# Optimization experiments

Measured on AMD Instinct MI355X. Metric: run time of the kernel, lower is better.

Reference implementation:

```python
import jax, jax.numpy as jnp
import numpy as np

# Deformable DETR encoder layer constants (match init_kwargs / input_specs)
SPATIAL_SHAPES = [(100, 152), (50, 76), (25, 38), (13, 19)]  # (H, W) per level
D_MODEL, D_FFN = 256, 1024
N_LEVELS, N_HEADS, N_POINTS = 4, 8, 4
HEAD_DIM = D_MODEL // N_HEADS
LEN_IN = sum(h * w for h, w in SPATIAL_SHAPES)  # 20197
BATCH = 2


def layer_norm(x, g, b, eps=1e-5):
    m = x.mean(-1, keepdims=True)
    v = ((x - m) ** 2).mean(-1, keepdims=True)
    return (x - m) * jax.lax.rsqrt(v + eps) * g + b


def sample_level(value_l, loc, H, W):
    # value_l: [B, nH, H*W, d]; loc: [B, nH, N, 2] normalized to [0,1]
    # Bilinear sampling, align_corners=False, zero padding (torch grid_sample semantics)
    x = loc[..., 0] * W - 0.5
    y = loc[..., 1] * H - 0.5
    x0, y0 = jnp.floor(x), jnp.floor(y)
    out = jnp.zeros(loc.shape[:-1] + (value_l.shape[-1],), value_l.dtype)
    for dx, dy in ((0, 0), (1, 0), (0, 1), (1, 1)):
        xi, yi = x0 + dx, y0 + dy
        w = (1.0 - jnp.abs(x - xi)) * (1.0 - jnp.abs(y - yi))
        valid = (xi >= 0) & (xi < W) & (yi >= 0) & (yi < H)
        idx = (jnp.clip(yi, 0, H - 1) * W + jnp.clip(xi, 0, W - 1)).astype(jnp.int32)
        v = jnp.take_along_axis(value_l, idx[..., None], axis=2)  # [B,nH,N,d]
        out = out + v * (w * valid.astype(value_l.dtype))[..., None]
    return out


def ms_deform_attn(query, src, ref, W_off, b_off, W_attn, b_attn, W_val, b_val, W_out, b_out):
    B, Lq, C = query.shape
    # value projection -> [B, nH, Len_in, head_dim]
    value = (src @ W_val + b_val).reshape(B, LEN_IN, N_HEADS, HEAD_DIM).transpose(0, 2, 1, 3)
    off = (query @ W_off + b_off).reshape(B, Lq, N_HEADS, N_LEVELS, N_POINTS, 2)
    attn = (query @ W_attn + b_attn).reshape(B, Lq, N_HEADS, N_LEVELS * N_POINTS)
    attn = jax.nn.softmax(attn, -1).reshape(B, Lq, N_HEADS, N_LEVELS, N_POINTS)
    # offset normalizer is (W, H) per level
    normalizer = jnp.array([[w, h] for h, w in SPATIAL_SHAPES], dtype=query.dtype)
    loc = ref[:, :, None, :, None, :] + off / normalizer[None, None, None, :, None, :]  # [B,Lq,nH,nL,nP,2]
    out = jnp.zeros((B, N_HEADS, Lq, HEAD_DIM), query.dtype)
    start = 0
    for l, (H, W) in enumerate(SPATIAL_SHAPES):
        v_l = value[:, :, start:start + H * W]
        start += H * W
        loc_l = loc[:, :, :, l].transpose(0, 2, 1, 3, 4).reshape(B, N_HEADS, Lq * N_POINTS, 2)
        s = sample_level(v_l, loc_l, H, W).reshape(B, N_HEADS, Lq, N_POINTS, HEAD_DIM)
        a = attn[:, :, :, l].transpose(0, 2, 1, 3)  # [B,nH,Lq,nP]
        out = out + (s * a[..., None]).sum(3)
    out = out.transpose(0, 2, 1, 3).reshape(B, Lq, C)
    return out @ W_out + b_out


def setup_inputs() -> dict:
    key = jax.random.key(0)
    ks = jax.random.split(key, 20)
    s = 0.02
    spatial_shapes = jnp.array(SPATIAL_SHAPES, dtype=jnp.int64)
    lsi = np.cumsum([0] + [h * w for h, w in SPATIAL_SHAPES[:-1]])
    return {
        'src': jax.random.normal(ks[0], (BATCH, LEN_IN, D_MODEL), jnp.float32),
        'pos': jax.random.normal(ks[1], (BATCH, LEN_IN, D_MODEL), jnp.float32),
        'reference_points': jax.random.uniform(ks[2], (BATCH, LEN_IN, N_LEVELS, 2), jnp.float32),
        'spatial_shapes': spatial_shapes,
        'level_start_index': jnp.array(lsi, dtype=jnp.int64),
        'W_off': jax.random.normal(ks[3], (D_MODEL, N_HEADS * N_LEVELS * N_POINTS * 2), jnp.float32) * s,
        'b_off': jax.random.normal(ks[4], (N_HEADS * N_LEVELS * N_POINTS * 2,), jnp.float32) * s,
        'W_attn': jax.random.normal(ks[5], (D_MODEL, N_HEADS * N_LEVELS * N_POINTS), jnp.float32) * s,
        'b_attn': jnp.zeros((N_HEADS * N_LEVELS * N_POINTS,), jnp.float32),
        'W_val': jax.random.normal(ks[6], (D_MODEL, D_MODEL), jnp.float32) * s,
        'b_val': jnp.zeros((D_MODEL,), jnp.float32),
        'W_out': jax.random.normal(ks[7], (D_MODEL, D_MODEL), jnp.float32) * s,
        'b_out': jnp.zeros((D_MODEL,), jnp.float32),
        'W1': jax.random.normal(ks[8], (D_MODEL, D_FFN), jnp.float32) * s,
        'b1': jnp.zeros((D_FFN,), jnp.float32),
        'W2': jax.random.normal(ks[9], (D_FFN, D_MODEL), jnp.float32) * s,
        'b2': jnp.zeros((D_MODEL,), jnp.float32),
        'g1': jnp.ones((D_MODEL,), jnp.float32),
        'be1': jnp.zeros((D_MODEL,), jnp.float32),
        'g2': jnp.ones((D_MODEL,), jnp.float32),
        'be2': jnp.zeros((D_MODEL,), jnp.float32),
    }


def reference(src, pos, reference_points, spatial_shapes, level_start_index,
              W_off, b_off, W_attn, b_attn, W_val, b_val, W_out, b_out,
              W1, b1, W2, b2, g1, be1, g2, be2):
    # eval mode: all dropouts are identity; ReLUDropout -> relu
    query = src + pos
    src2 = ms_deform_attn(query, src, reference_points,
                          W_off, b_off, W_attn, b_attn, W_val, b_val, W_out, b_out)
    x = layer_norm(src + src2, g1, be1)
    ffn = jax.nn.relu(x @ W1 + b1) @ W2 + b2
    return layer_norm(x + ffn, g2, be2)
```

## Files before the change

kernel.cpp:

```cpp
#include <hip/hip_runtime.h>
#include <math.h>

#define LEN_IN_C 20197
#define BATCH_C 2
#define BL_C (BATCH_C * LEN_IN_C)

typedef short  bf16x8 __attribute__((ext_vector_type(8)));
typedef float  f32x4  __attribute__((ext_vector_type(4)));

__device__ __forceinline__ ushort f2bf(float f) {
    unsigned u = __float_as_uint(f);
    return (ushort)((u + 0x7fffu + ((u >> 16) & 1u)) >> 16);
}
__device__ __forceinline__ float bf2f(ushort u) {
    return __uint_as_float((uint)u << 16);
}
__device__ __forceinline__ uint pkbf(float a, float b) {
    uint r;
    asm("v_cvt_pk_bf16_f32 %0, %1, %2" : "=v"(r) : "v"(a), "v"(b));
    return r;
}
__device__ __forceinline__ void dot2bf(float& a, uint v, uint w) {
    asm("v_dot2_f32_bf16 %0, %1, %2, %0" : "+v"(a) : "v"(v), "v"(w));
}
__device__ __forceinline__ void gload16(const void* g, void* l) {
    __builtin_amdgcn_global_load_lds(
        (const __attribute__((address_space(1))) unsigned char*)g,
        (__attribute__((address_space(3))) unsigned char*)l, 16, 0, 0);
}
__device__ __forceinline__ int xcd_swz(int lid, int nwg) {
    const int q = nwg >> 3, r = nwg & 7;
    const int xcd = lid & 7, p = lid >> 3;
    return (xcd < r ? xcd * (q + 1) : r * (q + 1) + (xcd - r) * q) + p;
}

__device__ __forceinline__ void tcast32(
    const float* W, ushort* WT, int K, int N, int n0, int k0, float* tile )
{
    const int ty = threadIdx.x >> 3, tx = threadIdx.x & 7;
    float4 v = *(const float4*)(W + (size_t)(k0 + ty) * N + n0 + tx * 4);
    tile[ty * 33 + tx * 4 + 0] = v.x; tile[ty * 33 + tx * 4 + 1] = v.y;
    tile[ty * 33 + tx * 4 + 2] = v.z; tile[ty * 33 + tx * 4 + 3] = v.w;
    __syncthreads();
    ushort4 o;
    o.x = f2bf(tile[(tx * 4 + 0) * 33 + ty]);
    o.y = f2bf(tile[(tx * 4 + 1) * 33 + ty]);
    o.z = f2bf(tile[(tx * 4 + 2) * 33 + ty]);
    o.w = f2bf(tile[(tx * 4 + 3) * 33 + ty]);
    *(ushort4*)(WT + (size_t)(n0 + ty) * K + k0 + tx * 4) = o;
}

__global__ __launch_bounds__(256) void prep_all(
    const float* __restrict__ src, const float* __restrict__ pos,
    const float* __restrict__ Wv, const float* __restrict__ Wo,
    const float* __restrict__ Wa, const float* __restrict__ Wout,
    const float* __restrict__ W1, const float* __restrict__ W2,
    const float* __restrict__ bo, const float* __restrict__ ba,
    ushort* __restrict__ Tval, ushort* __restrict__ Toa,
    ushort* __restrict__ Tout, ushort* __restrict__ TW1,
    ushort* __restrict__ TW2, float* __restrict__ boa,
    ushort* __restrict__ qout, ushort* __restrict__ srcb)
{
    __shared__ float tile[32 * 33];
    const int bx = blockIdx.x;
    const int tid = threadIdx.x;
    if (bx < 64) {
        tcast32(Wv, Tval, 256, 256, (bx & 7) * 32, (bx >> 3) * 32, tile);
    } else if (bx < 128) {
        const int s = bx - 64;
        tcast32(Wout, Tout, 256, 256, (s & 7) * 32, (s >> 3) * 32, tile);
    } else if (bx < 384) {
        const int s = bx - 128;
        tcast32(W1, TW1, 256, 1024, (s & 31) * 32, (s >> 5) * 32, tile);
    } else if (bx < 640) {
        const int s = bx - 384;
        tcast32(W2, TW2, 1024, 256, (s & 7) * 32, (s >> 3) * 32, tile);
    } else if (bx < 736) {
        const int idx = (bx - 640) * 256 + tid;
        const int n = idx >> 6, k4 = (idx & 63) * 4;
        ushort4 o; ushort* po = (ushort*)&o;
        #pragma unroll
        for (int j = 0; j < 4; ++j) {
            const int k = k4 + j;
            const float v = (n < 256) ? Wo[(size_t)k * 256 + n]
                                      : Wa[(size_t)k * 128 + (n - 256)];
            po[j] = f2bf(v);
        }
        *(ushort4*)(Toa + (size_t)n * 256 + k4) = o;
    } else if (bx < 738) {
        const int n = (bx - 736) * 256 + tid;
        if (n < 384) boa[n] = (n < 256) ? bo[n] : ba[n - 256];
    } else {
        const int n8 = BL_C * 32;
        for (int i = (bx - 738) * 256 + tid; i < n8; i += 1024 * 256) {
            const size_t base = (size_t)i * 8;
            float4 a0 = *(const float4*)(src + base);
            float4 a1 = *(const float4*)(src + base + 4);
            float4 b0 = *(const float4*)(pos + base);
            float4 b1 = *(const float4*)(pos + base + 4);
            uint4 o;
            o.x = pkbf(a0.x + b0.x, a0.y + b0.y);
            o.y = pkbf(a0.z + b0.z, a0.w + b0.w);
            o.z = pkbf(a1.x + b1.x, a1.y + b1.y);
            o.w = pkbf(a1.z + b1.z, a1.w + b1.w);
            *(uint4*)(qout + base) = o;
            uint4 s4;
            s4.x = pkbf(a0.x, a0.y); s4.y = pkbf(a0.z, a0.w);
            s4.z = pkbf(a1.x, a1.y); s4.w = pkbf(a1.z, a1.w);
            *(uint4*)(srcb + base) = s4;
        }
    }
}

template <bool RELU>
__device__ __forceinline__ void gemm_core(
    ushort* lsB, const int lid,
    const ushort* __restrict__ A, const ushort* __restrict__ BT,
    const float* __restrict__ bias, ushort* __restrict__ C,
    const int M, const int N, const int K, const int NT, const int nwg)
{
    const int nid = xcd_swz(lid, nwg);
    const int nt = nid % NT, mt = nid / NT;
    const int row0 = mt * 128, col0 = nt * 64;

    const int tid = threadIdx.x;
    const int ln = tid & 63, wv = tid >> 6;
    const int l16 = ln & 15, lk = ln >> 4;

    uint abase[2];
    #pragma unroll
    for (int m = 0; m < 2; ++m) {
        int rr = row0 + wv * 32 + m * 16 + l16;
        if (rr > M - 1) rr = M - 1;
        abase[m] = (uint)rr * K + lk * 8;
    }
    uint bbase[4], bxor[4];
    #pragma unroll
    for (int n = 0; n < 4; ++n) {
        const int brow = n * 16 + l16;
        bbase[n] = (uint)(brow * 256 + lk * 16);
        bxor[n]  = (uint)((brow & 7) << 4);
    }

    f32x4 acc[2][4] = {};
    const int nch = K >> 7;

    for (int ch = 0; ch < nch; ++ch) {
        const int kc0 = ch << 7;

        bf16x8 ar[4][2];
        #pragma unroll
        for (int s = 0; s < 4; ++s)
            #pragma unroll
            for (int m = 0; m < 2; ++m)
                ar[s][m] = *(const bf16x8*)(A + abase[m] + kc0 + s * 32);

        if (ch) __syncthreads();
        #pragma unroll
        for (int j = 0; j < 4; ++j) {
            const int d = j * 256 + tid;
            const int brow = d >> 4;
            const int c = (d & 15) ^ (brow & 7);
            gload16(BT + (size_t)(col0 + brow) * K + kc0 + c * 8,
                    (char*)lsB + j * 4096 + wv * 1024);
        }
        __syncthreads();

        #pragma unroll
        for (int gs = 0; gs < 4; ++gs) {
            bf16x8 bv[4];
            #pragma unroll
            for (int n = 0; n < 4; ++n)
                bv[n] = *(const bf16x8*)((const char*)lsB +
                        ((bbase[n] + gs * 64) ^ bxor[n]));
            #pragma unroll
            for (int m = 0; m < 2; ++m)
                #pragma unroll
                for (int n = 0; n < 4; ++n)
                    acc[m][n] = __builtin_amdgcn_mfma_f32_16x16x32_bf16(
                        bv[n], ar[gs][m], acc[m][n], 0, 0, 0);
        }
    }

    #pragma unroll
    for (int m = 0; m < 2; ++m) {
        const int grow = row0 + wv * 32 + m * 16 + l16;
        if (grow >= M) continue;
        ushort* crow = C + (size_t)grow * N;
        #pragma unroll
        for (int n = 0; n < 4; ++n) {
            const int col4 = col0 + n * 16 + lk * 4;
            float4 bs = *(const float4*)(bias + col4);
            f32x4 v = acc[m][n];
            float o0 = v[0] + bs.x, o1 = v[1] + bs.y, o2 = v[2] + bs.z, o3 = v[3] + bs.w;
            if (RELU) {
                o0 = fmaxf(o0, 0.f); o1 = fmaxf(o1, 0.f);
                o2 = fmaxf(o2, 0.f); o3 = fmaxf(o3, 0.f);
            }
            *(uint2*)(crow + col4) = make_uint2(pkbf(o0, o1), pkbf(o2, o3));
        }
    }
}

template <bool RELU>
__global__ __launch_bounds__(256) void gemm_bs(
    const ushort* __restrict__ A, const ushort* __restrict__ BT,
    const float* __restrict__ bias, ushort* __restrict__ C,
    const int M, const int N, const int K, const int NT, const int nwg)
{
    __shared__ ushort lsB[64 * 128];
    gemm_core<RELU>(lsB, blockIdx.x, A, BT, bias, C, M, N, K, NT, nwg);
}

__global__ __launch_bounds__(256) void gemm_dual(
    const ushort* __restrict__ A1, const ushort* __restrict__ BT1,
    const float* __restrict__ b1, ushort* __restrict__ C1,
    const int N1, const int NT1, const int nwg1,
    const ushort* __restrict__ A2, const ushort* __restrict__ BT2,
    const float* __restrict__ b2, ushort* __restrict__ C2,
    const int N2, const int NT2, const int nwg2)
{
    __shared__ ushort lsB[64 * 128];
    if ((int)blockIdx.x < nwg1)
        gemm_core<false>(lsB, blockIdx.x, A1, BT1, b1, C1, BL_C, N1, 256, NT1, nwg1);
    else
        gemm_core<false>(lsB, blockIdx.x - nwg1, A2, BT2, b2, C2, BL_C, N2, 256, NT2, nwg2);
}

__global__ __launch_bounds__(256) void sample_kernel(
    const ushort* __restrict__ value,
    const ushort* __restrict__ oa,
    const float* __restrict__ ref,
    ushort* __restrict__ outbf)
{
    constexpr int Hs[4] = {100, 50, 25, 13};
    constexpr int Ws[4] = {152, 76, 38, 19};
    constexpr int St[4] = {0, 15200, 19000, 19950};
    constexpr int NWG = (BL_C + 7) / 8;

    const int bq0 = xcd_swz(blockIdx.x, NWG) * 8;
    const int t = threadIdx.x;

    __shared__ uint2 s_pw[8][8][33];

    #pragma unroll
    for (int rnd = 0; rnd < 4; ++rnd) {
        const int qi2 = t >> 7, r2 = t & 127;
        const int qloc = rnd * 2 + qi2;
        int bq = bq0 + qloc; if (bq > BL_C - 1) bq = BL_C - 1;
        const int b = (bq >= LEN_IN_C) ? 1 : 0;
        const int h = r2 >> 4, i = r2 & 15, l = i >> 2, p = i & 3;
        const ushort* crow = oa + (size_t)bq * 384;

        float lg = bf2f(crow[256 + h * 16 + i]);
        float mx = lg;
        #pragma unroll
        for (int o = 1; o < 16; o <<= 1) mx = fmaxf(mx, __shfl_xor(mx, o, 16));
        float e = __expf(lg - mx), sm = e;
        #pragma unroll
        for (int o = 1; o < 16; o <<= 1) sm += __shfl_xor(sm, o, 16);
        const float aw = e / sm;

        const uint ov = *(const uint*)(crow + h * 32 + l * 8 + p * 2);
        const float ox = __uint_as_float(ov << 16);
        const float oy = __uint_as_float(ov & 0xffff0000u);
        const float2 rxy = *(const float2*)(ref + (size_t)bq * 8 + l * 2);
        const int H = Hs[l], W = Ws[l];
        const float x = rxy.x * (float)W + ox - 0.5f;
        const float y = rxy.y * (float)H + oy - 0.5f;
        const float x0f = floorf(x), y0f = floorf(y);
        const float fx = x - x0f, fy = y - y0f;
        const int x0 = (int)x0f, y0 = (int)y0f;

        const float wx0 = (x0 >= 0 && x0 < W) ? (1.f - fx) : 0.f;
        const float wx1 = (x0 + 1 >= 0 && x0 + 1 < W) ? fx : 0.f;
        int xb = x0 < 0 ? 0 : (x0 > W - 2 ? W - 2 : x0);
        float wLx = (xb == x0) ? wx0 : ((xb == x0 + 1) ? wx1 : 0.f);
        float wRx = (xb + 1 == x0 + 1) ? wx1 : ((xb + 1 == x0) ? wx0 : 0.f);
        wLx *= aw; wRx *= aw;

        const uint rowb = (uint)(b * LEN_IN_C + St[l] + xb);
        #pragma unroll
        for (int dy = 0; dy < 2; ++dy) {
            const int yy = y0 + dy;
            const bool vy = (yy >= 0) & (yy < H);
            const float wy = vy ? (dy ? fy : 1.f - fy) : 0.f;
            const int yc = yy < 0 ? 0 : (yy > H - 1 ? H - 1 : yy);
            const uint off = (rowb + (uint)(yc * W)) * 512u;
            s_pw[qloc][h][i * 2 + dy] = make_uint2(off, pkbf(wRx * wy, wLx * wy));
        }
    }
    __syncthreads();

    const int q = t >> 5, h2 = (t >> 2) & 7, d4 = t & 3;
    int bq = bq0 + q; if (bq > BL_C - 1) bq = BL_C - 1;
    const char* vb = (const char*)value;
    const uint toff = (uint)(h2 * 64 + d4 * 16);

    float a0 = 0.f, a1 = 0.f, a2 = 0.f, a3 = 0.f;
    float a4 = 0.f, a5 = 0.f, a6 = 0.f, a7 = 0.f;
    #pragma unroll 4
    for (int j = 0; j < 32; ++j) {
        const uint2 pw = s_pw[q][h2][j];
        const char* p = vb + (size_t)(pw.x + toff);
        const uint4 v0 = *(const uint4*)p;
        const uint4 v1 = *(const uint4*)(p + 512);
        const uint w = pw.y;
        dot2bf(a0, __builtin_amdgcn_perm(v0.x, v1.x, 0x05040100u), w);
        dot2bf(a1, __builtin_amdgcn_perm(v0.x, v1.x, 0x07060302u), w);
        dot2bf(a2, __builtin_amdgcn_perm(v0.y, v1.y, 0x05040100u), w);
        dot2bf(a3, __builtin_amdgcn_perm(v0.y, v1.y, 0x07060302u), w);
        dot2bf(a4, __builtin_amdgcn_perm(v0.z, v1.z, 0x05040100u), w);
        dot2bf(a5, __builtin_amdgcn_perm(v0.z, v1.z, 0x07060302u), w);
        dot2bf(a6, __builtin_amdgcn_perm(v0.w, v1.w, 0x05040100u), w);
        dot2bf(a7, __builtin_amdgcn_perm(v0.w, v1.w, 0x07060302u), w);
    }
    uint4 o;
    o.x = pkbf(a0, a1); o.y = pkbf(a2, a3);
    o.z = pkbf(a4, a5); o.w = pkbf(a6, a7);
    *(uint4*)(outbf + (size_t)bq * 256 + h2 * 32 + d4 * 8) = o;
}

template <bool ABF, bool OF32>
__global__ __launch_bounds__(256) void add_ln(
    const void* __restrict__ ap, const ushort* __restrict__ bp,
    const float* __restrict__ g, const float* __restrict__ be,
    void* __restrict__ op)
{
    const int row = blockIdx.x * 4 + (threadIdx.x >> 6);
    if (row >= BL_C) return;
    const int ln = threadIdx.x & 63;
    const size_t base = (size_t)row * 256 + ln * 4;

    float x[4];
    if (ABF) {
        ushort4 a4 = *(const ushort4*)((const ushort*)ap + base);
        x[0] = bf2f(a4.x); x[1] = bf2f(a4.y); x[2] = bf2f(a4.z); x[3] = bf2f(a4.w);
    } else {
        float4 a4 = *(const float4*)((const float*)ap + base);
        x[0] = a4.x; x[1] = a4.y; x[2] = a4.z; x[3] = a4.w;
    }
    ushort4 b4 = *(const ushort4*)(bp + base);
    x[0] += bf2f(b4.x); x[1] += bf2f(b4.y); x[2] += bf2f(b4.z); x[3] += bf2f(b4.w);

    float s = x[0] + x[1] + x[2] + x[3];
    #pragma unroll
    for (int o = 32; o >= 1; o >>= 1) s += __shfl_xor(s, o, 64);
    const float mean = s * (1.f / 256.f);
    float d0 = x[0] - mean, d1 = x[1] - mean, d2 = x[2] - mean, d3 = x[3] - mean;
    float ss = d0 * d0 + d1 * d1 + d2 * d2 + d3 * d3;
    #pragma unroll
    for (int o = 32; o >= 1; o >>= 1) ss += __shfl_xor(ss, o, 64);
    const float rs = rsqrtf(ss * (1.f / 256.f) + 1e-5f);

    float4 gv = *(const float4*)(g + ln * 4);
    float4 bv = *(const float4*)(be + ln * 4);
    float o0 = d0 * rs * gv.x + bv.x;
    float o1 = d1 * rs * gv.y + bv.y;
    float o2 = d2 * rs * gv.z + bv.z;
    float o3 = d3 * rs * gv.w + bv.w;

    if (OF32) {
        *(float4*)((float*)op + base) = make_float4(o0, o1, o2, o3);
    } else {
        ushort4 st;
        st.x = f2bf(o0); st.y = f2bf(o1); st.z = f2bf(o2); st.w = f2bf(o3);
        *(ushort4*)((ushort*)op + base) = st;
    }
}

extern "C" void kernel_launch(void* const* d_in, const int* in_sizes, int n_in,
                              void* d_out, int out_size, void* d_ws, size_t ws_size,
                              hipStream_t stream) {
    const float* src    = (const float*)d_in[0];
    const float* pos    = (const float*)d_in[1];
    const float* refpts = (const float*)d_in[2];
    const float* W_off  = (const float*)d_in[5];
    const float* b_off  = (const float*)d_in[6];
    const float* W_attn = (const float*)d_in[7];
    const float* b_attn = (const float*)d_in[8];
    const float* W_val  = (const float*)d_in[9];
    const float* b_val  = (const float*)d_in[10];
    const float* W_out  = (const float*)d_in[11];
    const float* b_out  = (const float*)d_in[12];
    const float* W1     = (const float*)d_in[13];
    const float* b1     = (const float*)d_in[14];
    const float* W2     = (const float*)d_in[15];
    const float* b2     = (const float*)d_in[16];
    const float* g1     = (const float*)d_in[17];
    const float* be1    = (const float*)d_in[18];
    const float* g2     = (const float*)d_in[19];
    const float* be2    = (const float*)d_in[20];
    float* out = (float*)d_out;
    (void)in_sizes; (void)n_in; (void)out_size; (void)ws_size;

    const int BL = BL_C;
    char* ws = (char*)d_ws;
    const size_t HB  = (size_t)BL * 256 * 2;
    const size_t OAB = (size_t)BL * 384 * 2;

    ushort* q_bf    = (ushort*)(ws);
    ushort* x_bf    = (ushort*)(ws);
    ushort* val_bf  = (ushort*)(ws + HB);
    ushort* oa_bf   = (ushort*)(ws + 2 * HB);
    ushort* ao_bf   = (ushort*)(ws + 2 * HB + OAB);
    ushort* src2_bf = (ushort*)(ws + 3 * HB + OAB);
    ushort* srcb_bf = (ushort*)(ws + 4 * HB + OAB);
    ushort* ffn2_bf = srcb_bf;
    ushort* mid_bf  = val_bf;
    char*   wts     = ws + 5 * HB + OAB;
    ushort* Tval = (ushort*)(wts);
    ushort* Toa  = Tval + 256 * 256;
    ushort* Tout = Toa + 384 * 256;
    ushort* TW1  = Tout + 256 * 256;
    ushort* TW2  = TW1 + 1024 * 256;
    float*  boa  = (float*)(TW2 + 256 * 1024);

    dim3 blk(256);
    const int MT = (BL + 127) / 128;

    prep_all<<<dim3(738 + 1024), blk, 0, stream>>>(
        src, pos, W_val, W_off, W_attn, W_out, W1, W2, b_off, b_attn,
        Tval, Toa, Tout, TW1, TW2, boa, q_bf, srcb_bf);

    gemm_dual<<<dim3(MT * 4 + MT * 6), blk, 0, stream>>>(
        srcb_bf, Tval, b_val, val_bf, 256, 4, MT * 4,
        q_bf, Toa, boa, oa_bf, 384, 6, MT * 6);

    sample_kernel<<<dim3((BL + 7) / 8), blk, 0, stream>>>(val_bf, oa_bf, refpts, ao_bf);

    gemm_bs<false><<<dim3(MT * 4), blk, 0, stream>>>(
        ao_bf, Tout, b_out, src2_bf, BL, 256, 256, 4, MT * 4);

    add_ln<true, false><<<dim3((BL + 3) / 4), blk, 0, stream>>>(
        srcb_bf, src2_bf, g1, be1, x_bf);

    gemm_bs<true><<<dim3(MT * 16), blk, 0, stream>>>(
        x_bf, TW1, b1, mid_bf, BL, 1024, 256, 16, MT * 16);

    gemm_bs<false><<<dim3(MT * 4), blk, 0, stream>>>(
        mid_bf, TW2, b2, ffn2_bf, BL, 256, 1024, 4, MT * 4);

    add_ln<true, true><<<dim3((BL + 3) / 4), blk, 0, stream>>>(
        x_bf, ffn2_bf, g2, be2, out);
}
```

Before: 290.0 us.

## Double-buffer GEMM B tiles in LDS and prefetch A registers

Restructures the GEMM main loop into a two-stage software pipeline. While the current chunk is computed, the B tile for the next K chunk is loaded into a second LDS buffer and the next A fragments are loaded into a second register set. Explicit vmcnt waits and raw barriers replace the per-chunk __syncthreads pairs. This is meant to hide global load latency behind MFMA work, at the cost of twice the LDS, more registers, and possible lower occupancy.

```diff
diff --git a/kernel.cpp b/kernel.cpp
--- a/kernel.cpp
+++ b/kernel.cpp
@@ -27,6 +27,12 @@
     __builtin_amdgcn_global_load_lds(
         (const __attribute__((address_space(1))) unsigned char*)g,
         (__attribute__((address_space(3))) unsigned char*)l, 16, 0, 0);
+}
+__device__ __forceinline__ void wait_vm12() {
+    asm volatile("s_waitcnt vmcnt(12)" ::: "memory");
+}
+__device__ __forceinline__ void wait_vm0() {
+    asm volatile("s_waitcnt vmcnt(0)" ::: "memory");
 }
 __device__ __forceinline__ int xcd_swz(int lid, int nwg) {
     const int q = nwg >> 3, r = nwg & 7;
@@ -114,7 +120,8 @@
 
 template <bool RELU>
 __device__ __forceinline__ void gemm_core(
-    ushort* lsB, const int lid,
+    char* lsB,
+    const int lid,
     const ushort* __restrict__ A, const ushort* __restrict__ BT,
     const float* __restrict__ bias, ushort* __restrict__ C,
     const int M, const int N, const int K, const int NT, const int nwg)
@@ -145,40 +152,59 @@
     f32x4 acc[2][4] = {};
     const int nch = K >> 7;
 
-    for (int ch = 0; ch < nch; ++ch) {
+    bf16x8 rA[4][2], rB[4][2];
+
+    auto stage = [&](int ch, int bufsel) {
         const int kc0 = ch << 7;
-
-        bf16x8 ar[4][2];
-        #pragma unroll
-        for (int s = 0; s < 4; ++s)
-            #pragma unroll
-            for (int m = 0; m < 2; ++m)
-                ar[s][m] = *(const bf16x8*)(A + abase[m] + kc0 + s * 32);
-
-        if (ch) __syncthreads();
         #pragma unroll
         for (int j = 0; j < 4; ++j) {
             const int d = j * 256 + tid;
             const int brow = d >> 4;
             const int c = (d & 15) ^ (brow & 7);
             gload16(BT + (size_t)(col0 + brow) * K + kc0 + c * 8,
-                    (char*)lsB + j * 4096 + wv * 1024);
-        }
-        __syncthreads();
-
+                    lsB + bufsel * 16384 + j * 4096 + wv * 1024);
+        }
+    };
+    auto pref = [&](int ch, bf16x8 (&ring)[4][2]) {
+        const int kc0 = ch << 7;
+        #pragma unroll
+        for (int s = 0; s < 4; ++s)
+            #pragma unroll
+            for (int m = 0; m < 2; ++m)
+                ring[s][m] = *(const bf16x8*)(A + abase[m] + kc0 + s * 32);
+    };
+    auto compute = [&](int bufsel, bf16x8 (&ring)[4][2]) {
         #pragma unroll
         for (int gs = 0; gs < 4; ++gs) {
             bf16x8 bv[4];
             #pragma unroll
             for (int n = 0; n < 4; ++n)
-                bv[n] = *(const bf16x8*)((const char*)lsB +
+                bv[n] = *(const bf16x8*)(lsB + bufsel * 16384 +
                         ((bbase[n] + gs * 64) ^ bxor[n]));
             #pragma unroll
             for (int m = 0; m < 2; ++m)
                 #pragma unroll
                 for (int n = 0; n < 4; ++n)
                     acc[m][n] = __builtin_amdgcn_mfma_f32_16x16x32_bf16(
-                        bv[n], ar[gs][m], acc[m][n], 0, 0, 0);
+                        bv[n], ring[gs][m], acc[m][n], 0, 0, 0);
+        }
+    };
+
+    stage(0, 0); pref(0, rA);
+    for (int c = 0; c < nch; c += 2) {
+        const bool h1 = (c + 1 < nch);
+        if (h1) { stage(c + 1, 1); pref(c + 1, rB); }
+        if (h1) wait_vm12(); else wait_vm0();
+        __builtin_amdgcn_s_barrier();
+        compute(0, rA);
+        __builtin_amdgcn_s_barrier();
+        if (h1) {
+            const bool h2 = (c + 2 < nch);
+            if (h2) { stage(c + 2, 0); pref(c + 2, rA); }
+            if (h2) wait_vm12(); else wait_vm0();
+            __builtin_amdgcn_s_barrier();
+            compute(1, rB);
+            __builtin_amdgcn_s_barrier();
         }
     }
 
@@ -208,7 +234,7 @@
     const float* __restrict__ bias, ushort* __restrict__ C,
     const int M, const int N, const int K, const int NT, const int nwg)
 {
-    __shared__ ushort lsB[64 * 128];
+    __shared__ __align__(16) char lsB[32768];
     gemm_core<RELU>(lsB, blockIdx.x, A, BT, bias, C, M, N, K, NT, nwg);
 }
 
@@ -220,7 +246,7 @@
     const float* __restrict__ b2, ushort* __restrict__ C2,
     const int N2, const int NT2, const int nwg2)
 {
-    __shared__ ushort lsB[64 * 128];
+    __shared__ __align__(16) char lsB[32768];
     if ((int)blockIdx.x < nwg1)
         gemm_core<false>(lsB, blockIdx.x, A1, BT1, b1, C1, BL_C, N1, 256, NT1, nwg1);
     else
```

Measured after the change: 293.8 us. No clear change (+1.3%).
